# Kernel optimization log

Measured on AMD Instinct MI355X. Metric: run time of the kernel, lower is better.

The kernel has to match this reference:

```python
import jax, jax.numpy as jnp
import numpy as np

B, V, C, H, W, D = 2, 3, 8, 128, 160, 64


def bilinear_sample(feat, grid):
    """feat: [B,C,H,W]; grid: [B,N,2] normalized to [-1,1], align_corners=True,
    padding_mode='zeros' (matches F.grid_sample). Returns [B,C,N]."""
    b, c, h, w = feat.shape
    ix = (grid[..., 0] + 1.0) * 0.5 * (w - 1)  # [B,N]
    iy = (grid[..., 1] + 1.0) * 0.5 * (h - 1)
    x0 = jnp.floor(ix)
    y0 = jnp.floor(iy)
    wx1 = ix - x0
    wy1 = iy - y0
    flat = feat.reshape(b, c, h * w)

    def corner(xi, yi, wgt):
        valid = (xi >= 0) & (xi <= w - 1) & (yi >= 0) & (yi <= h - 1)
        xc = jnp.clip(xi, 0, w - 1).astype(jnp.int32)
        yc = jnp.clip(yi, 0, h - 1).astype(jnp.int32)
        idx = yc * w + xc  # [B,N]
        vals = jnp.take_along_axis(flat, jnp.broadcast_to(idx[:, None, :], (b, c, idx.shape[1])), axis=2)
        return vals * (wgt * valid.astype(feat.dtype))[:, None, :]

    out = (corner(x0, y0, (1 - wx1) * (1 - wy1))
           + corner(x0 + 1, y0, wx1 * (1 - wy1))
           + corner(x0, y0 + 1, (1 - wx1) * wy1)
           + corner(x0 + 1, y0 + 1, wx1 * wy1))
    return out


def homo_warping(src_feat, proj_mat, depth_values):
    """src_feat [B,C,H,W], proj_mat [B,3,4], depth_values [B,D,H,W].
    Returns warped volume [B,C,D,H,W] and normalized grid [B,D,H,W,2]."""
    b, c, h, w = src_feat.shape
    d = depth_values.shape[1]
    R = proj_mat[:, :, :3]
    T = proj_mat[:, :, 3:]  # [B,3,1]
    ys, xs = jnp.meshgrid(jnp.arange(h, dtype=src_feat.dtype),
                          jnp.arange(w, dtype=src_feat.dtype), indexing='ij')
    ref = jnp.stack([xs.ravel(), ys.ravel(), jnp.ones(h * w, src_feat.dtype)], 0)  # [3,HW]
    Rp = jnp.einsum('bij,jp->bip', R, ref)  # [B,3,HW]
    dv = depth_values.reshape(b, d, h * w)
    src = Rp[:, :, None, :] + T[:, :, :, None] / dv[:, None, :, :]  # [B,3,D,HW]
    xy = src[:, :2] / src[:, 2:3]
    gx = xy[:, 0] / ((w - 1) / 2.0) - 1.0
    gy = xy[:, 1] / ((h - 1) / 2.0) - 1.0
    grid = jnp.stack([gx, gy], axis=-1)  # [B,D,HW,2]
    warped = bilinear_sample(src_feat, grid.reshape(b, d * h * w, 2)).reshape(b, c, d, h, w)
    return warped, grid.reshape(b, d, h, w, 2)


def setup_inputs() -> dict:
    key = jax.random.key(0)
    k1, k2, k3, k4, k5 = jax.random.split(key, 5)
    features = jax.random.normal(k1, (V, B, C, H, W), dtype=jnp.float32)
    # near-identity projective maps so warps land mostly in-bounds
    eye = jnp.broadcast_to(jnp.eye(3, dtype=jnp.float32), (B, V, 3, 3))
    Rm = eye + 0.01 * jax.random.normal(k2, (B, V, 3, 3), dtype=jnp.float32)
    Tm = 2.0 * jax.random.normal(k3, (B, V, 3, 1), dtype=jnp.float32)
    proj_matrices = jnp.concatenate([Rm, Tm], axis=-1)  # [B,V,3,4]
    base = jnp.linspace(2.0, 10.0, D, dtype=jnp.float32)[None, :, None, None]
    depth_values = base + 0.1 * jax.random.uniform(k4, (B, D, H, W), dtype=jnp.float32)
    reg_weight = jax.random.normal(k5, (C,), dtype=jnp.float32)
    return {"features": features, "proj_matrices": proj_matrices,
            "depth_values": depth_values, "reg_weight": reg_weight,
            "num_depth": D}


def reference(features, proj_matrices, depth_values, reg_weight, num_depth):
    v = features.shape[0]
    ref_feat = features[0]
    b, c, h, w = ref_feat.shape
    d = num_depth
    ref_volume = jnp.broadcast_to(ref_feat[:, :, None], (b, c, d, h, w))
    volume_sum = ref_volume
    volume_sq_sum = ref_volume ** 2
    in_masks = jnp.ones((b, 1, d, h, w), dtype=ref_feat.dtype)
    for i in range(1, v):  # fixed small number of source views
        warped, grid = homo_warping(features[i], proj_matrices[:, i], depth_values)
        m = (grid > -1.0) & (grid < 1.0)
        in_masks = in_masks + (m[..., 0] & m[..., 1]).astype(ref_feat.dtype)[:, None]
        volume_sum = volume_sum + warped
        volume_sq_sum = volume_sq_sum + warped ** 2
    count = 1.0 / in_masks
    volume_feat = volume_sq_sum * count - (volume_sum * count) ** 2  # [B,C,D,H,W]
    # stand-in cost regularization: channel reduction -> [B,D,H,W]
    cost = jnp.einsum('bcdhw,c->bdhw', volume_feat, reg_weight)
    prob_volume = jax.nn.softmax(cost, axis=1)
    depth = jnp.sum(prob_volume * depth_values, axis=1)  # [B,H,W]
    return depth
```

## Files before the change

kernel.cpp:

```cpp
#include <hip/hip_runtime.h>
#include <math.h>

#define BB 2
#define VV 3
#define CC 8
#define HH 128
#define WW 160
#define DD 64
constexpr int HW = HH * WW;
constexpr int NPIX = BB * HW;
constexpr int PX_PER_BLOCK = 32;
constexpr int CHUNKS = 8;
constexpr int DPC = DD / CHUNKS;

typedef _Float16 h8 __attribute__((ext_vector_type(8)));

static __device__ __forceinline__ h8 splat8(float x) {
    const _Float16 v = (_Float16)x;
    h8 r = {v, v, v, v, v, v, v, v};
    return r;
}

__global__ __launch_bounds__(256)
void transpose_feats(const float* __restrict__ feats, h8* __restrict__ ft)
{
    const int t = blockIdx.x * blockDim.x + threadIdx.x;
    if (t >= VV * BB * HW) return;
    const int vb = t / HW;
    const int hw = t - vb * HW;
    const float* src = feats + (size_t)vb * CC * HW + hw;
    h8 v;
#pragma unroll
    for (int c = 0; c < CC; ++c) v[c] = (_Float16)src[(size_t)c * HW];
    ft[(size_t)vb * HW + hw] = v;
}

__global__ __launch_bounds__(256)
void depthnet_fused(const h8* __restrict__ ft,
                    const float* __restrict__ proj,
                    const float* __restrict__ depthv,
                    const float* __restrict__ regw,
                    float* __restrict__ out)
{
    __shared__ float sm_m[4 * PX_PER_BLOCK];
    __shared__ float sm_l[4 * PX_PER_BLOCK];
    __shared__ float sm_s[4 * PX_PER_BLOCK];

    const int tid   = threadIdx.x;
    const int lane  = tid & 63;
    const int wave  = tid >> 6;
    const int px    = lane & 31;
    const int sub   = lane >> 5;
    const int chunk = wave * 2 + sub;
    const int pixel = blockIdx.x * PX_PER_BLOCK + px;

    const int b  = (pixel >= HW) ? 1 : 0;
    const int hw = pixel - b * HW;
    const int h  = hw / WW;
    const int w  = hw - h * WW;

    float rf[CC], rf2[CC];
    {
        h8 rv = ft[(size_t)b * HW + hw];
#pragma unroll
        for (int c = 0; c < CC; ++c) { rf[c] = (float)rv[c]; rf2[c] = rf[c] * rf[c]; }
    }

    float Rp[2][3], Tv[2][3];
    const float xf = (float)w, yf = (float)h;
#pragma unroll
    for (int v = 0; v < 2; ++v) {
        const float* M = proj + ((size_t)b * VV + (v + 1)) * 12;
#pragma unroll
        for (int j = 0; j < 3; ++j) {
            Rp[v][j] = M[j * 4 + 0] * xf + M[j * 4 + 1] * yf + M[j * 4 + 2];
            Tv[v][j] = M[j * 4 + 3];
        }
    }

    const h8* fsrc0 = ft + (size_t)(1 * BB + b) * HW;
    const h8* fsrc1 = ft + (size_t)(2 * BB + b) * HW;

    const float* dvp = depthv + (size_t)b * DD * HW + hw;
    float dvv[DPC];
#pragma unroll
    for (int k = 0; k < DPC; ++k) dvv[k] = dvp[(size_t)(chunk * DPC + k) * HW];

    float cost[DPC];
    h8 A0, A1, A2, A3, B0, B1, B2, B3;
    int pa0 = 0, pa3 = 0, pb0 = 0, pb3 = 0;

#pragma unroll
    for (int k = 0; k < DPC; ++k) {
        const float d = dvv[k];

        float wt[2][4];
        int   ib[2][4];
        float nmask = 1.0f;
#pragma unroll
        for (int v = 0; v < 2; ++v) {
            const float sx = Rp[v][0] * d + Tv[v][0];
            const float sy = Rp[v][1] * d + Tv[v][1];
            const float sz = Rp[v][2] * d + Tv[v][2];
            const float rsz = __builtin_amdgcn_rcpf(sz);
            const float ix = sx * rsz;
            const float iy = sy * rsz;
            nmask += ((ix > 0.f) && (ix < (float)(WW - 1)) &&
                      (iy > 0.f) && (iy < (float)(HH - 1))) ? 1.0f : 0.0f;
            const float x0f = floorf(ix), y0f = floorf(iy);
            const float wx1 = ix - x0f, wy1 = iy - y0f;
            const float wx0 = 1.f - wx1, wy0 = 1.f - wy1;
            const float x1f = x0f + 1.f, y1f = y0f + 1.f;
            const bool vx0 = (x0f >= 0.f) && (x0f <= (float)(WW - 1));
            const bool vx1 = (x1f >= 0.f) && (x1f <= (float)(WW - 1));
            const bool vy0 = (y0f >= 0.f) && (y0f <= (float)(HH - 1));
            const bool vy1 = (y1f >= 0.f) && (y1f <= (float)(HH - 1));
            wt[v][0] = wx0 * wy0 * ((vx0 && vy0) ? 1.f : 0.f);
            wt[v][1] = wx1 * wy0 * ((vx1 && vy0) ? 1.f : 0.f);
            wt[v][2] = wx0 * wy1 * ((vx0 && vy1) ? 1.f : 0.f);
            wt[v][3] = wx1 * wy1 * ((vx1 && vy1) ? 1.f : 0.f);
            const int x0c = (int)fminf(fmaxf(x0f, 0.f), (float)(WW - 1));
            const int x1c = (int)fminf(fmaxf(x1f, 0.f), (float)(WW - 1));
            const int y0c = (int)fminf(fmaxf(y0f, 0.f), (float)(HH - 1));
            const int y1c = (int)fminf(fmaxf(y1f, 0.f), (float)(HH - 1));
            ib[v][0] = y0c * WW + x0c;
            ib[v][1] = y0c * WW + x1c;
            ib[v][2] = y1c * WW + x0c;
            ib[v][3] = y1c * WW + x1c;
        }

        if (k == 0) {
            A0 = fsrc0[ib[0][0]]; A1 = fsrc0[ib[0][1]];
            A2 = fsrc0[ib[0][2]]; A3 = fsrc0[ib[0][3]];
            B0 = fsrc1[ib[1][0]]; B1 = fsrc1[ib[1][1]];
            B2 = fsrc1[ib[1][2]]; B3 = fsrc1[ib[1][3]];
        } else {
            if (ib[0][0] != pa0 || ib[0][3] != pa3) {
                A0 = fsrc0[ib[0][0]]; A1 = fsrc0[ib[0][1]];
                A2 = fsrc0[ib[0][2]]; A3 = fsrc0[ib[0][3]];
            }
            if (ib[1][0] != pb0 || ib[1][3] != pb3) {
                B0 = fsrc1[ib[1][0]]; B1 = fsrc1[ib[1][1]];
                B2 = fsrc1[ib[1][2]]; B3 = fsrc1[ib[1][3]];
            }
        }
        pa0 = ib[0][0]; pa3 = ib[0][3];
        pb0 = ib[1][0]; pb3 = ib[1][3];

        h8 vah = A0 * splat8(wt[0][0]) + A1 * splat8(wt[0][1])
               + A2 * splat8(wt[0][2]) + A3 * splat8(wt[0][3]);
        h8 vbh = B0 * splat8(wt[1][0]) + B1 * splat8(wt[1][1])
               + B2 * splat8(wt[1][2]) + B3 * splat8(wt[1][3]);

        const float cnt = __builtin_amdgcn_rcpf(nmask);
        float t1 = 0.f, t2 = 0.f;
#pragma unroll
        for (int c = 0; c < CC; ++c) {
            const float av = (float)vah[c];
            const float bv = (float)vbh[c];
            const float sum = rf[c] + av + bv;
            const float sq  = rf2[c] + av * av + bv * bv;
            t1 += regw[c] * sq;
            t2 += (regw[c] * sum) * sum;
        }
        cost[k] = cnt * t1 - (cnt * cnt) * t2;
    }

    float m = cost[0];
#pragma unroll
    for (int k = 1; k < DPC; ++k) m = fmaxf(m, cost[k]);
    float l = 0.f, s = 0.f;
#pragma unroll
    for (int k = 0; k < DPC; ++k) {
        const float e = __expf(cost[k] - m);
        l += e;
        s += e * dvv[k];
    }

    {
        const float m2 = __shfl_xor(m, 32, 64);
        const float l2 = __shfl_xor(l, 32, 64);
        const float s2 = __shfl_xor(s, 32, 64);
        const float M  = fmaxf(m, m2);
        const float e1 = __expf(m - M);
        const float e2 = __expf(m2 - M);
        l = l * e1 + l2 * e2;
        s = s * e1 + s2 * e2;
        m = M;
    }

    if (lane < PX_PER_BLOCK) {
        sm_m[wave * PX_PER_BLOCK + px] = m;
        sm_l[wave * PX_PER_BLOCK + px] = l;
        sm_s[wave * PX_PER_BLOCK + px] = s;
    }
    __syncthreads();

    if (tid < PX_PER_BLOCK) {
        float M = sm_m[tid], L = sm_l[tid], S = sm_s[tid];
#pragma unroll
        for (int wv = 1; wv < 4; ++wv) {
            const float m2 = sm_m[wv * PX_PER_BLOCK + tid];
            const float l2 = sm_l[wv * PX_PER_BLOCK + tid];
            const float s2 = sm_s[wv * PX_PER_BLOCK + tid];
            const float Mn = fmaxf(M, m2);
            const float e1 = __expf(M - Mn);
            const float e2 = __expf(m2 - Mn);
            L = L * e1 + l2 * e2;
            S = S * e1 + s2 * e2;
            M = Mn;
        }
        out[blockIdx.x * PX_PER_BLOCK + tid] = S / L;
    }
}

extern "C" void kernel_launch(void* const* d_in, const int* in_sizes, int n_in,
                              void* d_out, int out_size, void* d_ws, size_t ws_size,
                              hipStream_t stream) {
    const float* feats  = (const float*)d_in[0];
    const float* proj   = (const float*)d_in[1];
    const float* depthv = (const float*)d_in[2];
    const float* regw   = (const float*)d_in[3];
    float* out = (float*)d_out;
    h8* ft = (h8*)d_ws;

    {
        const int n = VV * BB * HW;
        hipLaunchKernelGGL(transpose_feats, dim3((n + 255) / 256), dim3(256), 0, stream,
                           feats, ft);
    }
    {
        const int grid = NPIX / PX_PER_BLOCK;
        hipLaunchKernelGGL(depthnet_fused, dim3(grid), dim3(256), 0, stream,
                           ft, proj, depthv, regw, out);
    }
}
```

Before: 108.7 us.

## Split depth across more threads per pixel and swizzle blocks across XCDs

Each block now covers 16 pixels instead of 32, and each thread handles 4 depth samples instead of 8, so 16 lanes share a pixel's depth range. The softmax partials are merged with a two-step xor-shuffle butterfly before the shared-memory combine. Block indices are remapped so that consecutive blocks on the same XCD cover contiguous pixels, which should improve L2 locality for the gathers. The aims are more parallelism and shorter per-thread serial chains. In exchange, per-pixel setup is repeated more often and there is less reuse of cached corner loads across depths.

```diff
diff --git a/kernel.cpp b/kernel.cpp
--- a/kernel.cpp
+++ b/kernel.cpp
@@ -9,9 +9,10 @@
 #define DD 64
 constexpr int HW = HH * WW;
 constexpr int NPIX = BB * HW;
-constexpr int PX_PER_BLOCK = 32;
-constexpr int CHUNKS = 8;
-constexpr int DPC = DD / CHUNKS;
+constexpr int PX_PER_BLOCK = 16;
+constexpr int DPT = 4;
+constexpr int GRID_FUSED = NPIX / PX_PER_BLOCK;
+constexpr int XCD_STRIDE = GRID_FUSED / 8;
 
 typedef _Float16 h8 __attribute__((ext_vector_type(8)));
 
@@ -49,10 +50,12 @@
     const int tid   = threadIdx.x;
     const int lane  = tid & 63;
     const int wave  = tid >> 6;
-    const int px    = lane & 31;
-    const int sub   = lane >> 5;
-    const int chunk = wave * 2 + sub;
-    const int pixel = blockIdx.x * PX_PER_BLOCK + px;
+    const int px    = lane & 15;
+    const int sub   = lane >> 4;
+    const int chunk = wave * 4 + sub;
+    const int d0    = chunk * DPT;
+    const int bswz  = (blockIdx.x & 7) * XCD_STRIDE + (blockIdx.x >> 3);
+    const int pixel = bswz * PX_PER_BLOCK + px;
 
     const int b  = (pixel >= HW) ? 1 : 0;
     const int hw = pixel - b * HW;
@@ -82,16 +85,16 @@
     const h8* fsrc1 = ft + (size_t)(2 * BB + b) * HW;
 
     const float* dvp = depthv + (size_t)b * DD * HW + hw;
-    float dvv[DPC];
-#pragma unroll
-    for (int k = 0; k < DPC; ++k) dvv[k] = dvp[(size_t)(chunk * DPC + k) * HW];
-
-    float cost[DPC];
+    float dvv[DPT];
+#pragma unroll
+    for (int k = 0; k < DPT; ++k) dvv[k] = dvp[(size_t)(d0 + k) * HW];
+
+    float cost[DPT];
     h8 A0, A1, A2, A3, B0, B1, B2, B3;
-    int pa0 = 0, pa3 = 0, pb0 = 0, pb3 = 0;
-
-#pragma unroll
-    for (int k = 0; k < DPC; ++k) {
+    int pa0 = -1, pa3 = -1, pb0 = -1, pb3 = -1;
+
+#pragma unroll
+    for (int k = 0; k < DPT; ++k) {
         const float d = dvv[k];
 
         float wt[2][4];
@@ -129,23 +132,16 @@
             ib[v][3] = y1c * WW + x1c;
         }
 
-        if (k == 0) {
+        if (ib[0][0] != pa0 || ib[0][3] != pa3) {
             A0 = fsrc0[ib[0][0]]; A1 = fsrc0[ib[0][1]];
             A2 = fsrc0[ib[0][2]]; A3 = fsrc0[ib[0][3]];
+            pa0 = ib[0][0]; pa3 = ib[0][3];
+        }
+        if (ib[1][0] != pb0 || ib[1][3] != pb3) {
             B0 = fsrc1[ib[1][0]]; B1 = fsrc1[ib[1][1]];
             B2 = fsrc1[ib[1][2]]; B3 = fsrc1[ib[1][3]];
-        } else {
-            if (ib[0][0] != pa0 || ib[0][3] != pa3) {
-                A0 = fsrc0[ib[0][0]]; A1 = fsrc0[ib[0][1]];
-                A2 = fsrc0[ib[0][2]]; A3 = fsrc0[ib[0][3]];
-            }
-            if (ib[1][0] != pb0 || ib[1][3] != pb3) {
-                B0 = fsrc1[ib[1][0]]; B1 = fsrc1[ib[1][1]];
-                B2 = fsrc1[ib[1][2]]; B3 = fsrc1[ib[1][3]];
-            }
-        }
-        pa0 = ib[0][0]; pa3 = ib[0][3];
-        pb0 = ib[1][0]; pb3 = ib[1][3];
+            pb0 = ib[1][0]; pb3 = ib[1][3];
+        }
 
         h8 vah = A0 * splat8(wt[0][0]) + A1 * splat8(wt[0][1])
                + A2 * splat8(wt[0][2]) + A3 * splat8(wt[0][3]);
@@ -166,21 +162,20 @@
         cost[k] = cnt * t1 - (cnt * cnt) * t2;
     }
 
-    float m = cost[0];
-#pragma unroll
-    for (int k = 1; k < DPC; ++k) m = fmaxf(m, cost[k]);
+    float m = fmaxf(fmaxf(cost[0], cost[1]), fmaxf(cost[2], cost[3]));
     float l = 0.f, s = 0.f;
 #pragma unroll
-    for (int k = 0; k < DPC; ++k) {
+    for (int k = 0; k < DPT; ++k) {
         const float e = __expf(cost[k] - m);
         l += e;
         s += e * dvv[k];
     }
 
-    {
-        const float m2 = __shfl_xor(m, 32, 64);
-        const float l2 = __shfl_xor(l, 32, 64);
-        const float s2 = __shfl_xor(s, 32, 64);
+#pragma unroll
+    for (int off = 16; off < 64; off <<= 1) {
+        const float m2 = __shfl_xor(m, off, 64);
+        const float l2 = __shfl_xor(l, off, 64);
+        const float s2 = __shfl_xor(s, off, 64);
         const float M  = fmaxf(m, m2);
         const float e1 = __expf(m - M);
         const float e2 = __expf(m2 - M);
@@ -210,7 +205,7 @@
             S = S * e1 + s2 * e2;
             M = Mn;
         }
-        out[blockIdx.x * PX_PER_BLOCK + tid] = S / L;
+        out[bswz * PX_PER_BLOCK + tid] = S / L;
     }
 }
 
@@ -230,8 +225,7 @@
                            feats, ft);
     }
     {
-        const int grid = NPIX / PX_PER_BLOCK;
-        hipLaunchKernelGGL(depthnet_fused, dim3(grid), dim3(256), 0, stream,
+        hipLaunchKernelGGL(depthnet_fused, dim3(GRID_FUSED), dim3(256), 0, stream,
                            ft, proj, depthv, regw, out);
     }
 }
```

After: 96.27 us, median of 2. -11.4%, faster.
